# Performance work log

Measured on AMD Instinct MI355X. Metric: run time of the kernel, lower is better.

Reference implementation:

```python
import jax, jax.numpy as jnp
import numpy as np

# Standard bitsandbytes NF4 codebook (16 values)
NF4_CODE = jnp.array([
    -1.0, -0.6961928009986877, -0.5250730514526367, -0.39491748809814453,
    -0.28444138169288635, -0.18477343022823334, -0.09105003625154495, 0.0,
    0.07958029955625534, 0.16093020141124725, 0.24611230194568634,
    0.33791524171829224, 0.44070982933044434, 0.5626170039176941,
    0.7229568362236023, 1.0], dtype=jnp.float32)

BLOCKSIZE = 64
IN_FEATURES = 4096
OUT_FEATURES = 11008


def setup_inputs() -> dict:
    key = jax.random.key(0)
    k1, k2, k3, k4 = jax.random.split(key, 4)
    x = jax.random.normal(k1, (4, 2048, IN_FEATURES), dtype=jnp.float32)
    weight_q = jax.random.randint(k2, (OUT_FEATURES, IN_FEATURES), 0, 16, dtype=jnp.int32)
    absmax = jax.random.uniform(k3, (OUT_FEATURES, IN_FEATURES // BLOCKSIZE), dtype=jnp.float32)
    bias = jax.random.normal(k4, (OUT_FEATURES,), dtype=jnp.float32)
    return {"x": x, "weight_q": weight_q, "absmax": absmax, "bias": bias}


def reference(x, weight_q, absmax, bias):
    out_f, in_f = weight_q.shape
    # Blockwise NF4 dequantization: code lookup * per-block absmax scale
    w_code = NF4_CODE[weight_q]                                   # [O, I]
    w_blocks = w_code.reshape(out_f, in_f // BLOCKSIZE, BLOCKSIZE)
    w = (w_blocks * absmax[:, :, None]).reshape(out_f, in_f)      # [O, I]
    # Linear: y = x @ W^T + b
    y = jnp.einsum('bsi,oi->bso', x, w) + bias
    return y
```

## Files before the change

kernel.cpp:

```cpp
#include <hip/hip_runtime.h>
#include <hip/hip_bf16.h>
#include <stdint.h>

typedef __attribute__((ext_vector_type(8))) short short8;
typedef __attribute__((ext_vector_type(8))) unsigned short ushort8;
typedef __attribute__((ext_vector_type(4))) float f32x4;

#define K_DIM 4096
#define N_DIM 11008
#define M_DIM 8192
#define BM 256
#define BN 256
#define BK 64
#define TILES (K_DIM / BK)

__constant__ float c_nf4[16] = {
    -1.0f, -0.6961928009986877f, -0.5250730514526367f, -0.39491748809814453f,
    -0.28444138169288635f, -0.18477343022823334f, -0.09105003625154495f, 0.0f,
    0.07958029955625534f, 0.16093020141124725f, 0.24611230194568634f,
    0.33791524171829224f, 0.44070982933044434f, 0.5626170039176941f,
    0.7229568362236023f, 1.0f};

__device__ __forceinline__ unsigned short f2bf(float f) {
    uint32_t u = __float_as_uint(f);
    u += 0x7fffu + ((u >> 16) & 1u);
    return (unsigned short)(u >> 16);
}

__global__ __launch_bounds__(256) void nf4_dequant_w(const int* __restrict__ q,
                                                     const float* __restrict__ absmax,
                                                     unsigned short* __restrict__ w) {
    __shared__ float lut[16];
    if (threadIdx.x < 16) lut[threadIdx.x] = c_nf4[threadIdx.x];
    __syncthreads();
    size_t t = (size_t)blockIdx.x * 256 + threadIdx.x;
    const int4* q4 = (const int4*)q;
    int4 qa = q4[2 * t];
    int4 qb = q4[2 * t + 1];
    float s = absmax[t >> 3];
    ushort8 o;
    o[0] = f2bf(lut[qa.x & 15] * s);
    o[1] = f2bf(lut[qa.y & 15] * s);
    o[2] = f2bf(lut[qa.z & 15] * s);
    o[3] = f2bf(lut[qa.w & 15] * s);
    o[4] = f2bf(lut[qb.x & 15] * s);
    o[5] = f2bf(lut[qb.y & 15] * s);
    o[6] = f2bf(lut[qb.z & 15] * s);
    o[7] = f2bf(lut[qb.w & 15] * s);
    ((ushort8*)w)[t] = o;
}

__global__ __launch_bounds__(256) void x_to_bf16(const float* __restrict__ x,
                                                 unsigned short* __restrict__ xb) {
    size_t t = (size_t)blockIdx.x * 256 + threadIdx.x;
    const float4* x4 = (const float4*)x;
    float4 a = x4[2 * t];
    float4 b = x4[2 * t + 1];
    ushort8 o;
    o[0] = f2bf(a.x); o[1] = f2bf(a.y); o[2] = f2bf(a.z); o[3] = f2bf(a.w);
    o[4] = f2bf(b.x); o[5] = f2bf(b.y); o[6] = f2bf(b.z); o[7] = f2bf(b.w);
    ((ushort8*)xb)[t] = o;
}

#define STAGE_SUB(gbase, lds_sub, kcol0)                                      \
  do {                                                                        \
    _Pragma("unroll")                                                         \
    for (int _g = 0; _g < 2; ++_g) {                                          \
      const int _i = _g * 512 + tid;                             \
      const int _r = _i >> 2;                                 \
      const int _c = (_i & 3) << 3;                   \
      __builtin_amdgcn_global_load_lds(                                       \
          (const __attribute__((address_space(1))) void*)((gbase) +           \
              (size_t)_r * K_DIM + (kcol0) + _c),                             \
          (__attribute__((address_space(3))) void*)((lds_sub) +               \
              (_g * 512 + wave * 64) * 8),                                    \
          16, 0, 0);                                                          \
    }                                                                         \
  } while (0)

#define DS_A4(sub, rbase)                                                     \
  af[0] = *(const short8*)((sub) + ((rbase) +  0 + lr) * 32 + q8);            \
  af[1] = *(const short8*)((sub) + ((rbase) + 16 + lr) * 32 + q8);            \
  af[2] = *(const short8*)((sub) + ((rbase) + 32 + lr) * 32 + q8);            \
  af[3] = *(const short8*)((sub) + ((rbase) + 48 + lr) * 32 + q8);

#define DS_B4(sub)                                                            \
  bfr[0] = *(const short8*)((sub) + (wn * 64 +  0 + lr) * 32 + q8);           \
  bfr[1] = *(const short8*)((sub) + (wn * 64 + 16 + lr) * 32 + q8);           \
  bfr[2] = *(const short8*)((sub) + (wn * 64 + 32 + lr) * 32 + q8);           \
  bfr[3] = *(const short8*)((sub) + (wn * 64 + 48 + lr) * 32 + q8);

#define MFMA16(MI0)                                                           \
  do {                                                                        \
    _Pragma("unroll")                                                         \
    for (int _m = 0; _m < 4; ++_m) {                                          \
      _Pragma("unroll")                                                       \
      for (int _n = 0; _n < 4; ++_n)                                          \
        acc[(MI0) + _m][_n] = __builtin_amdgcn_mfma_f32_16x16x32_bf16(        \
            af[_m], bfr[_n], acc[(MI0) + _m][_n], 0, 0, 0);                   \
    }                                                                         \
  } while (0)

#define MIDBAR_MFMA(MI0)                                                      \
  asm volatile("s_barrier" ::: "memory");                                     \
  asm volatile("s_waitcnt lgkmcnt(0)" ::: "memory");                          \
  __builtin_amdgcn_sched_barrier(0);                                          \
  __builtin_amdgcn_s_setprio(1);                                              \
  MFMA16(MI0);                                                                \
  __builtin_amdgcn_s_setprio(0);                                              \
  __builtin_amdgcn_sched_barrier(0);                                          \
  asm volatile("s_barrier" ::: "memory");

__global__ __launch_bounds__(512, 2) void gemm256(const unsigned short* __restrict__ A,
                                                  const unsigned short* __restrict__ B,
                                                  const float* __restrict__ bias,
                                                  float* __restrict__ C) {
    __shared__ unsigned short As[2][2][BM * 32];
    __shared__ unsigned short Bs[2][2][BN * 32];

    const int tid  = threadIdx.x;
    const int wave = tid >> 6;
    const int lane = tid & 63;
    const int wm = wave >> 2;
    const int wn = wave & 3;
    const int lr = lane & 15;
    const int q8 = (lane >> 4) << 3;

    const int nbn = N_DIM / BN;
    const int cpx = (int)gridDim.x >> 3;
    const int bid = (int)blockIdx.x;
    const int swz = (bid & 7) * cpx + (bid >> 3);
    const int bm = swz / nbn;
    const int bn = swz % nbn;

    const unsigned short* Ab = A + (size_t)bm * BM * K_DIM;
    const unsigned short* Bb = B + (size_t)bn * BN * K_DIM;

    f32x4 acc[8][4];
#pragma unroll
    for (int i = 0; i < 8; ++i)
#pragma unroll
        for (int j = 0; j < 4; ++j)
#pragma unroll
            for (int v = 0; v < 4; ++v) acc[i][j][v] = 0.0f;

    STAGE_SUB(Ab, &As[0][0][0], 0);
    STAGE_SUB(Bb, &Bs[0][0][0], 0);
    STAGE_SUB(Ab, &As[0][1][0], 32);
    STAGE_SUB(Bb, &Bs[0][1][0], 32);
    STAGE_SUB(Ab, &As[1][0][0], BK);
    STAGE_SUB(Bb, &Bs[1][0][0], BK);
    asm volatile("s_waitcnt vmcnt(4)" ::: "memory");
    asm volatile("s_barrier" ::: "memory");

    short8 af[4], bfr[4];

#pragma unroll 1
    for (int t = 0; t < TILES; ++t) {
        const int p = t & 1;
        int t1 = t + 1; if (t1 >= TILES) t1 -= TILES;
        int t2 = t + 2; if (t2 >= TILES) t2 -= TILES;
        const int p1 = t1 & 1;
        const int p2 = t2 & 1;

        DS_A4(&As[p][0][0], wm * 128);
        DS_B4(&Bs[p][0][0]);
        STAGE_SUB(Ab, &As[p1][1][0], t1 * BK + 32);
        MIDBAR_MFMA(0);

        DS_A4(&As[p][0][0], wm * 128 + 64);
        STAGE_SUB(Bb, &Bs[p1][1][0], t1 * BK + 32);
        asm volatile("s_waitcnt vmcnt(4)" ::: "memory");
        MIDBAR_MFMA(4);

        DS_A4(&As[p][1][0], wm * 128);
        DS_B4(&Bs[p][1][0]);
        STAGE_SUB(Ab, &As[p2][0][0], t2 * BK);
        MIDBAR_MFMA(0);

        DS_A4(&As[p][1][0], wm * 128 + 64);
        STAGE_SUB(Bb, &Bs[p2][0][0], t2 * BK);
        asm volatile("s_waitcnt vmcnt(4)" ::: "memory");
        MIDBAR_MFMA(4);
    }
    asm volatile("s_waitcnt vmcnt(0)" ::: "memory");

    const int row0 = bm * BM + wm * 128 + ((lane >> 4) << 2);
    const int col0 = bn * BN + wn * 64 + lr;
#pragma unroll
    for (int ni = 0; ni < 4; ++ni) {
        const int col = col0 + ni * 16;
        const float bv = bias[col];
#pragma unroll
        for (int mi = 0; mi < 8; ++mi) {
#pragma unroll
            for (int v = 0; v < 4; ++v) {
                C[(size_t)(row0 + mi * 16 + v) * N_DIM + col] = acc[mi][ni][v] + bv;
            }
        }
    }
}

extern "C" void kernel_launch(void* const* d_in, const int* in_sizes, int n_in,
                              void* d_out, int out_size, void* d_ws, size_t ws_size,
                              hipStream_t stream) {
    const float* x    = (const float*)d_in[0];
    const int*   wq   = (const int*)d_in[1];
    const float* am   = (const float*)d_in[2];
    const float* bias = (const float*)d_in[3];
    float* out = (float*)d_out;

    const size_t w_elems = (size_t)N_DIM * K_DIM;
    const size_t x_elems = (size_t)M_DIM * K_DIM;
    const size_t need = (w_elems + x_elems) * sizeof(unsigned short);
    if (ws_size < need) return;

    unsigned short* wbf = (unsigned short*)d_ws;
    unsigned short* xbf = wbf + w_elems;

    nf4_dequant_w<<<(int)(w_elems / 8 / 256), 256, 0, stream>>>(wq, am, wbf);
    x_to_bf16<<<(int)(x_elems / 8 / 256), 256, 0, stream>>>(x, xbf);

    const int grid = (M_DIM / BM) * (N_DIM / BN);
    gemm256<<<grid, 512, 0, stream>>>(xbf, wbf, bias, out);
}
```

Before: 945.3 us.

## Switch GEMM LDS to XOR-swizzled 64-wide layout with one barrier per tile

```diff
diff --git a/kernel.cpp b/kernel.cpp
--- a/kernel.cpp
+++ b/kernel.cpp
@@ -62,35 +62,36 @@
     ((ushort8*)xb)[t] = o;
 }
 
-#define STAGE_SUB(gbase, lds_sub, kcol0)                                      \
+#define STAGE_HALF(gbase, lds_half, row0, k0)                                 \
   do {                                                                        \
     _Pragma("unroll")                                                         \
     for (int _g = 0; _g < 2; ++_g) {                                          \
-      const int _i = _g * 512 + tid;                             \
-      const int _r = _i >> 2;                                 \
-      const int _c = (_i & 3) << 3;                   \
+      const int _i = _g * 512 + tid;                        \
+      const int _r = _i >> 3;                           \
+      const int _c = (_i & 7) ^ (_r & 7);                   \
       __builtin_amdgcn_global_load_lds(                                       \
           (const __attribute__((address_space(1))) void*)((gbase) +           \
-              (size_t)_r * K_DIM + (kcol0) + _c),                             \
-          (__attribute__((address_space(3))) void*)((lds_sub) +               \
+              (size_t)((row0) + _r) * K_DIM + (k0) + _c * 8),                 \
+          (__attribute__((address_space(3))) void*)((lds_half) +              \
               (_g * 512 + wave * 64) * 8),                                    \
           16, 0, 0);                                                          \
     }                                                                         \
   } while (0)
 
-#define DS_A4(sub, rbase)                                                     \
-  af[0] = *(const short8*)((sub) + ((rbase) +  0 + lr) * 32 + q8);            \
-  af[1] = *(const short8*)((sub) + ((rbase) + 16 + lr) * 32 + q8);            \
-  af[2] = *(const short8*)((sub) + ((rbase) + 32 + lr) * 32 + q8);            \
-  af[3] = *(const short8*)((sub) + ((rbase) + 48 + lr) * 32 + q8);
-
-#define DS_B4(sub)                                                            \
-  bfr[0] = *(const short8*)((sub) + (wn * 64 +  0 + lr) * 32 + q8);           \
-  bfr[1] = *(const short8*)((sub) + (wn * 64 + 16 + lr) * 32 + q8);           \
-  bfr[2] = *(const short8*)((sub) + (wn * 64 + 32 + lr) * 32 + q8);           \
-  bfr[3] = *(const short8*)((sub) + (wn * 64 + 48 + lr) * 32 + q8);
+#define DS_A4(rbase, X)                                                       \
+  af[0] = *(const short8*)(Ah + ((rbase) +  0) * 64 + (roff ^ (X)));          \
+  af[1] = *(const short8*)(Ah + ((rbase) + 16) * 64 + (roff ^ (X)));          \
+  af[2] = *(const short8*)(Ah + ((rbase) + 32) * 64 + (roff ^ (X)));          \
+  af[3] = *(const short8*)(Ah + ((rbase) + 48) * 64 + (roff ^ (X)));
+
+#define DS_B4(X)                                                              \
+  bfr[0] = *(const short8*)(Bh + (bbase +  0) * 64 + (roff ^ (X)));           \
+  bfr[1] = *(const short8*)(Bh + (bbase + 16) * 64 + (roff ^ (X)));           \
+  bfr[2] = *(const short8*)(Bh + (bbase + 32) * 64 + (roff ^ (X)));           \
+  bfr[3] = *(const short8*)(Bh + (bbase + 48) * 64 + (roff ^ (X)));
 
 #define MFMA16(MI0)                                                           \
+  __builtin_amdgcn_s_setprio(1);                                              \
   do {                                                                        \
     _Pragma("unroll")                                                         \
     for (int _m = 0; _m < 4; ++_m) {                                          \
@@ -99,24 +100,15 @@
         acc[(MI0) + _m][_n] = __builtin_amdgcn_mfma_f32_16x16x32_bf16(        \
             af[_m], bfr[_n], acc[(MI0) + _m][_n], 0, 0, 0);                   \
     }                                                                         \
-  } while (0)
-
-#define MIDBAR_MFMA(MI0)                                                      \
-  asm volatile("s_barrier" ::: "memory");                                     \
-  asm volatile("s_waitcnt lgkmcnt(0)" ::: "memory");                          \
-  __builtin_amdgcn_sched_barrier(0);                                          \
-  __builtin_amdgcn_s_setprio(1);                                              \
-  MFMA16(MI0);                                                                \
-  __builtin_amdgcn_s_setprio(0);                                              \
-  __builtin_amdgcn_sched_barrier(0);                                          \
-  asm volatile("s_barrier" ::: "memory");
+  } while (0);                                                                \
+  __builtin_amdgcn_s_setprio(0);
 
 __global__ __launch_bounds__(512, 2) void gemm256(const unsigned short* __restrict__ A,
                                                   const unsigned short* __restrict__ B,
                                                   const float* __restrict__ bias,
                                                   float* __restrict__ C) {
-    __shared__ unsigned short As[2][2][BM * 32];
-    __shared__ unsigned short Bs[2][2][BN * 32];
+    __shared__ unsigned short As[2][2][128 * 64];
+    __shared__ unsigned short Bs[2][2][128 * 64];
 
     const int tid  = threadIdx.x;
     const int wave = tid >> 6;
@@ -124,7 +116,9 @@
     const int wm = wave >> 2;
     const int wn = wave & 3;
     const int lr = lane & 15;
-    const int q8 = (lane >> 4) << 3;
+    const int q  = lane >> 4;
+    const int roff = lr * 64 + ((q ^ (lr & 7)) << 3);
+    const int bbase = (wn & 1) * 64;
 
     const int nbn = N_DIM / BN;
     const int cpx = (int)gridDim.x >> 3;
@@ -144,13 +138,9 @@
 #pragma unroll
             for (int v = 0; v < 4; ++v) acc[i][j][v] = 0.0f;
 
-    STAGE_SUB(Ab, &As[0][0][0], 0);
-    STAGE_SUB(Bb, &Bs[0][0][0], 0);
-    STAGE_SUB(Ab, &As[0][1][0], 32);
-    STAGE_SUB(Bb, &Bs[0][1][0], 32);
-    STAGE_SUB(Ab, &As[1][0][0], BK);
-    STAGE_SUB(Bb, &Bs[1][0][0], BK);
-    asm volatile("s_waitcnt vmcnt(4)" ::: "memory");
+    STAGE_HALF(Ab, &As[0][0][0], 0,   0); STAGE_HALF(Bb, &Bs[0][0][0], 0,   0);
+    STAGE_HALF(Ab, &As[0][1][0], 128, 0); STAGE_HALF(Bb, &Bs[0][1][0], 128, 0);
+    asm volatile("s_waitcnt vmcnt(0)" ::: "memory");
     asm volatile("s_barrier" ::: "memory");
 
     short8 af[4], bfr[4];
@@ -158,34 +148,36 @@
 #pragma unroll 1
     for (int t = 0; t < TILES; ++t) {
         const int p = t & 1;
-        int t1 = t + 1; if (t1 >= TILES) t1 -= TILES;
-        int t2 = t + 2; if (t2 >= TILES) t2 -= TILES;
-        const int p1 = t1 & 1;
-        const int p2 = t2 & 1;
-
-        DS_A4(&As[p][0][0], wm * 128);
-        DS_B4(&Bs[p][0][0]);
-        STAGE_SUB(Ab, &As[p1][1][0], t1 * BK + 32);
-        MIDBAR_MFMA(0);
-
-        DS_A4(&As[p][0][0], wm * 128 + 64);
-        STAGE_SUB(Bb, &Bs[p1][1][0], t1 * BK + 32);
-        asm volatile("s_waitcnt vmcnt(4)" ::: "memory");
-        MIDBAR_MFMA(4);
-
-        DS_A4(&As[p][1][0], wm * 128);
-        DS_B4(&Bs[p][1][0]);
-        STAGE_SUB(Ab, &As[p2][0][0], t2 * BK);
-        MIDBAR_MFMA(0);
-
-        DS_A4(&As[p][1][0], wm * 128 + 64);
-        STAGE_SUB(Bb, &Bs[p2][0][0], t2 * BK);
-        asm volatile("s_waitcnt vmcnt(4)" ::: "memory");
-        MIDBAR_MFMA(4);
+        int t1 = t + 1; if (t1 >= TILES) t1 = 0;
+        const int k1 = t1 * BK;
+        const unsigned short* Ah = &As[p][wm][0];
+        const unsigned short* Bh = &Bs[p][wn >> 1][0];
+
+        DS_A4(0, 0);
+        DS_B4(0);
+        STAGE_HALF(Ab, &As[p ^ 1][0][0], 0, k1);
+        STAGE_HALF(Bb, &Bs[p ^ 1][0][0], 0, k1);
+        MFMA16(0);
+
+        DS_A4(64, 0);
+        STAGE_HALF(Ab, &As[p ^ 1][1][0], 128, k1);
+        STAGE_HALF(Bb, &Bs[p ^ 1][1][0], 128, k1);
+        MFMA16(4);
+
+        DS_A4(0, 32);
+        DS_B4(32);
+        MFMA16(0);
+
+        DS_A4(64, 32);
+        MFMA16(4);
+
+        asm volatile("s_waitcnt lgkmcnt(0)" ::: "memory");
+        __builtin_amdgcn_sched_barrier(0);
+        asm volatile("s_waitcnt vmcnt(0)" ::: "memory");
+        asm volatile("s_barrier" ::: "memory");
     }
-    asm volatile("s_waitcnt vmcnt(0)" ::: "memory");
-
-    const int row0 = bm * BM + wm * 128 + ((lane >> 4) << 2);
+
+    const int row0 = bm * BM + wm * 128 + (q << 2);
     const int col0 = bn * BN + wn * 64 + lr;
 #pragma unroll
     for (int ni = 0; ni < 4; ++ni) {
```

Measured after the change: 880.9 us. 1.07x faster.
